# Optimization experiments

Hardware: AMD Instinct MI355X
Metric: run time of the kernel (lower is better)

## Reference

```python
import jax, jax.numpy as jnp
import numpy as np

NUM_GROUPS = 32
EPS = 1e-5

def setup_inputs() -> dict:
    key = jax.random.key(0)
    ks = jax.random.split(key, 10)
    N, C, H, W = 4, 128, 64, 64
    x = jax.random.normal(ks[0], (N, C, H, W), dtype=jnp.float32)
    # GroupNorm affine params
    gn_scale = jnp.ones((C,), dtype=jnp.float32)
    gn_bias = jnp.zeros((C,), dtype=jnp.float32)
    # 1x1 conv weights [out, in] (xavier_uniform scale)
    lim = float(np.sqrt(6.0 / (C + C)))
    wq = jax.random.uniform(ks[1], (C, C), minval=-lim, maxval=lim, dtype=jnp.float32)
    wk = jax.random.uniform(ks[2], (C, C), minval=-lim, maxval=lim, dtype=jnp.float32)
    wv = jax.random.uniform(ks[3], (C, C), minval=-lim, maxval=lim, dtype=jnp.float32)
    wp = jax.random.uniform(ks[4], (C, C), minval=-lim, maxval=lim, dtype=jnp.float32) * 1e-5
    bq = jnp.zeros((C,), dtype=jnp.float32)
    bk = jnp.zeros((C,), dtype=jnp.float32)
    bv = jnp.zeros((C,), dtype=jnp.float32)
    bp = jnp.zeros((C,), dtype=jnp.float32)
    return {"x": x, "gn_scale": gn_scale, "gn_bias": gn_bias,
            "wq": wq, "bq": bq, "wk": wk, "bk": bk,
            "wv": wv, "bv": bv, "wp": wp, "bp": bp}

def _group_norm(x, scale, bias):
    # x: [N, C, H, W]
    N, C, H, W = x.shape
    g = x.reshape(N, NUM_GROUPS, C // NUM_GROUPS, H, W)
    mean = g.mean(axis=(2, 3, 4), keepdims=True)
    var = g.var(axis=(2, 3, 4), keepdims=True)
    g = (g - mean) * jax.lax.rsqrt(var + EPS)
    x = g.reshape(N, C, H, W)
    return x * scale[None, :, None, None] + bias[None, :, None, None]

def reference(x, gn_scale, gn_bias, wq, bq, wk, bk, wv, bv, wp, bp):
    N, C, H, W = x.shape
    h = _group_norm(x, gn_scale, gn_bias)
    # flatten spatial to tokens: [N, HW, C]
    ht = h.reshape(N, C, H * W).transpose(0, 2, 1)
    q = jnp.einsum('nlc,oc->nlo', ht, wq) + bq
    k = jnp.einsum('nlc,oc->nlo', ht, wk) + bk
    v = jnp.einsum('nlc,oc->nlo', ht, wv) + bv
    score = jnp.einsum('nqc,nkc->nqk', q, k) * (C ** -0.5)  # [N, HW, HW]
    attn = jax.nn.softmax(score, axis=-1)
    out = jnp.einsum('nqk,nkc->nqc', attn, v)  # [N, HW, C]
    out = jnp.einsum('nlc,oc->nlo', out, wp) + bp
    out = out.transpose(0, 2, 1).reshape(N, C, H, W)
    return x + out
```

## Files before the change

### kernel.cpp

```cpp
#include <hip/hip_runtime.h>

#define HW 4096
#define CCH 128
#define NB 4

typedef short bf16x8 __attribute__((ext_vector_type(8)));
typedef float f32x4 __attribute__((ext_vector_type(4)));

__device__ __forceinline__ unsigned short f2bf(float f){
  union { float fv; unsigned u; } v; v.fv = f;
  unsigned r = v.u + 0x7fffu + ((v.u >> 16) & 1u);
  return (unsigned short)(r >> 16);
}
__device__ __forceinline__ float bf2f(unsigned short u){
  return __uint_as_float(((unsigned)u) << 16);
}
__device__ __forceinline__ f32x4 mfma16(bf16x8 a, bf16x8 b, f32x4 c){
  return __builtin_amdgcn_mfma_f32_16x16x32_bf16(a, b, c, 0, 0, 0);
}
__device__ __forceinline__ void gll16(const void* g, void* l){
  __builtin_amdgcn_global_load_lds(
      (const __attribute__((address_space(1))) unsigned*)g,
      (__attribute__((address_space(3))) unsigned*)l, 16, 0, 0);
}

__global__ __launch_bounds__(256) void gn_stats_k(const float* __restrict__ x,
    float* __restrict__ stats,
    const float* __restrict__ wq, const float* __restrict__ wk,
    const float* __restrict__ wv, const float* __restrict__ wp,
    unsigned short* __restrict__ wqb, unsigned short* __restrict__ wkb,
    unsigned short* __restrict__ wvb, unsigned short* __restrict__ wpb){
  int tid = threadIdx.x;
  if (tid < 128){
    int f4 = blockIdx.x * 128 + tid;
    int m = f4 >> 12, e = f4 & 4095;
    const float* s4 = (m == 0) ? wq : ((m == 1) ? wk : ((m == 2) ? wv : wp));
    unsigned short* d4 = (m == 0) ? wqb : ((m == 1) ? wkb : ((m == 2) ? wvb : wpb));
    float4 v = *(const float4*)(s4 + e * 4);
    ushort4 b; b.x = f2bf(v.x); b.y = f2bf(v.y); b.z = f2bf(v.z); b.w = f2bf(v.w);
    *(ushort4*)(d4 + e * 4) = b;
  }
  int gid = blockIdx.x;
  const float4* p = (const float4*)(x + (size_t)gid * 16384);
  float s = 0.f, q = 0.f;
  #pragma unroll
  for (int i = 0; i < 16; i++){
    float4 v = p[tid + 256 * i];
    s += v.x + v.y + v.z + v.w;
    q += v.x * v.x + v.y * v.y + v.z * v.z + v.w * v.w;
  }
  #pragma unroll
  for (int d = 1; d < 64; d <<= 1){ s += __shfl_xor(s, d); q += __shfl_xor(q, d); }
  __shared__ float red[8];
  int w = tid >> 6;
  if ((tid & 63) == 0){ red[2 * w] = s; red[2 * w + 1] = q; }
  __syncthreads();
  if (tid == 0){
    float S = red[0] + red[2] + red[4] + red[6];
    float Q = red[1] + red[3] + red[5] + red[7];
    float mean = S * (1.f / 16384.f);
    float var  = Q * (1.f / 16384.f) - mean * mean;
    stats[2 * gid]     = mean;
    stats[2 * gid + 1] = rsqrtf(var + 1e-5f);
  }
}

__global__ __launch_bounds__(256) void gn_apply_k(const float* __restrict__ x,
    const float* __restrict__ stats, const float* __restrict__ sc,
    const float* __restrict__ bi, unsigned short* __restrict__ ht){
  int n = blockIdx.y, l0 = blockIdx.x * 32, tid = threadIdx.x;
  __shared__ __align__(16) unsigned short hs[32][136];
  #pragma unroll
  for (int i = 0; i < 16; i++){
    int c = (tid >> 5) + 8 * i;
    int l = tid & 31;
    float v = x[((size_t)(n * CCH + c)) * HW + l0 + l];
    int grp = n * 32 + (c >> 2);
    float r = (v - stats[2 * grp]) * stats[2 * grp + 1] * sc[c] + bi[c];
    hs[l][c] = f2bf(r);
  }
  __syncthreads();
  #pragma unroll
  for (int i = 0; i < 2; i++){
    int ch = tid + 256 * i;
    int l = ch >> 4, cb = (ch & 15) * 8;
    *(uint4*)&ht[((size_t)(n * HW) + l0 + l) * CCH + cb] = *(const uint4*)&hs[l][cb];
  }
}

__global__ __launch_bounds__(256, 3) void qkv_k(const unsigned short* __restrict__ ht,
    const unsigned short* __restrict__ wqb, const unsigned short* __restrict__ wkb,
    const unsigned short* __restrict__ wvb,
    const float* __restrict__ bq, const float* __restrict__ bk,
    const float* __restrict__ bv,
    unsigned short* __restrict__ Qg, unsigned short* __restrict__ Kg,
    unsigned short* __restrict__ Vt){
  int n = blockIdx.y, l0 = blockIdx.x * 64, m = blockIdx.z, tid = threadIdx.x;
  int w = tid >> 6, lane = tid & 63, l15 = lane & 15, g = lane >> 4;
  __shared__ __align__(16) char lds[49152];
  char* hA = lds;
  char* WB = lds + 16384;
  const unsigned short* wsrc = (m == 0) ? wqb : ((m == 1) ? wkb : wvb);
  const float* bsrc = (m == 0) ? bq : ((m == 1) ? bk : bv);
  {
    const char* hb = (const char*)ht + ((size_t)(n * HW) + l0) * (CCH * 2);
    #pragma unroll
    for (int i = 0; i < 4; i++){
      int T = (4 * w + i) * 64 + lane;
      int row = T >> 4, c16 = (T & 15) ^ (row & 15);
      gll16(hb + row * 256 + c16 * 16, hA + (4 * w + i) * 1024);
    }
    const char* wb2 = (const char*)wsrc;
    #pragma unroll
    for (int i = 0; i < 8; i++){
      int T = (8 * w + i) * 64 + lane;
      int row = T >> 4, c16 = (T & 15) ^ (row & 15);
      gll16(wb2 + row * 256 + c16 * 16, WB + (8 * w + i) * 1024);
    }
  }
  __syncthreads();
  bf16x8 a[4];
  #pragma unroll
  for (int kc = 0; kc < 4; kc++)
    a[kc] = *(const bf16x8*)(hA + (16 * w + l15) * 256 + ((4 * kc + g) ^ l15) * 16);
  f32x4 acc[8];
  #pragma unroll
  for (int ct = 0; ct < 8; ct++) acc[ct] = (f32x4)(0.f);
  #pragma unroll
  for (int ct = 0; ct < 8; ct++)
    #pragma unroll
    for (int kc = 0; kc < 4; kc++){
      bf16x8 bfr = *(const bf16x8*)(WB + (16 * ct + l15) * 256 + ((4 * kc + g) ^ l15) * 16);
      acc[ct] = mfma16(a[kc], bfr, acc[ct]);
    }
  __syncthreads();
  if (m < 2){
    float qs = (m == 0) ? 0.08838834764831845f : 1.0f;
    unsigned short* dst = (m == 0) ? Qg : Kg;
    unsigned short* os = (unsigned short*)(lds + 16384);
    #pragma unroll
    for (int ct = 0; ct < 8; ct++){
      int o = 16 * ct + l15;
      float bias = bsrc[o];
      #pragma unroll
      for (int r = 0; r < 4; r++)
        os[(16 * w + 4 * g + r) * 136 + o] = f2bf((acc[ct][r] + bias) * qs);
    }
    __syncthreads();
    #pragma unroll
    for (int i = 0; i < 4; i++){
      int T = tid + 256 * i;
      int row = T >> 4, cb = T & 15;
      *(uint4*)&dst[((size_t)(n * HW) + l0 + row) * CCH + cb * 8] =
          *(const uint4*)&os[row * 136 + cb * 8];
    }
  } else {
    unsigned short* os = (unsigned short*)(lds + 16384);
    #pragma unroll
    for (int ct = 0; ct < 8; ct++){
      int o = 16 * ct + l15;
      float bias = bsrc[o];
      #pragma unroll
      for (int r = 0; r < 4; r++)
        os[o * 72 + 16 * w + 4 * g + r] = f2bf(acc[ct][r] + bias);
    }
    __syncthreads();
    #pragma unroll
    for (int i = 0; i < 4; i++){
      int T = tid + 256 * i;
      int row = T >> 3, c = T & 7;
      *(uint4*)&Vt[((size_t)(n * CCH) + row) * HW + l0 + c * 8] =
          *(const uint4*)&os[row * 72 + c * 8];
    }
  }
}

__global__ __launch_bounds__(256, 2) void attn_k(const unsigned short* __restrict__ Qg,
    const unsigned short* __restrict__ Kg, const unsigned short* __restrict__ Vt,
    unsigned short* __restrict__ Op, float* __restrict__ Ml, int lsp){
  int nbk = gridDim.x, cpx = nbk >> 3, b = blockIdx.x;
  int swz = (b & 7) * cpx + (b >> 3);
  int q0 = (swz & 63) * 64;
  int rest = swz >> 6;
  int splits = 1 << lsp;
  int sp = rest & (splits - 1);
  int n = rest >> lsp;
  int kvs = HW >> lsp, nt = 64 >> lsp;
  int tid = threadIdx.x;
  int w = tid >> 6, lane = tid & 63, l15 = lane & 15, g = lane >> 4;
  __shared__ __align__(16) char lds[74752];
  char* Pw = lds + 65536 + w * 2304;

  bf16x8 qf[4];
  #pragma unroll
  for (int kc = 0; kc < 4; kc++)
    qf[kc] = *reinterpret_cast<const bf16x8*>(
        &Qg[((size_t)(n * HW) + q0 + 16 * w + l15) * CCH + 32 * kc + 8 * g]);
  f32x4 ov[8];
  #pragma unroll
  for (int i = 0; i < 8; i++) ov[i] = (f32x4)(0.f);
  float mrun[4] = {-3.0e38f, -3.0e38f, -3.0e38f, -3.0e38f};
  float lrun[4] = {0.f, 0.f, 0.f, 0.f};

  const char* kp[4]; const char* vp[4];
  {
    const char* kbase = (const char*)Kg + ((size_t)(n * HW) + sp * kvs) * (CCH * 2);
    const char* vbase = (const char*)Vt + (size_t)(n * CCH) * (HW * 2) + (size_t)sp * kvs * 2;
    #pragma unroll
    for (int i = 0; i < 4; i++){
      int C = (w * 4 + i) * 64 + lane;
      int row = C >> 4, c16 = (C & 15) ^ (row & 15);
      kp[i] = kbase + row * 256 + c16 * 16;
      int vrow = C >> 3, c8 = (C & 7) ^ (vrow & 7);
      vp[i] = vbase + (size_t)vrow * (HW * 2) + c8 * 16;
    }
  }

  #pragma unroll
  for (int i = 0; i < 4; i++) gll16(kp[i], lds + w * 4096 + i * 1024);
  #pragma unroll
  for (int i = 0; i < 4; i++) gll16(vp[i], lds + 16384 + w * 4096 + i * 1024);
  __syncthreads();

  for (int t = 0; t < nt; t++){
    char* cur = lds + ((t & 1) ? 32768 : 0);
    if (t + 1 < nt){
      char* nb = lds + ((t & 1) ? 0 : 32768);
      #pragma unroll
      for (int i = 0; i < 4; i++)
        gll16(kp[i] + (size_t)(t + 1) * 16384, nb + w * 4096 + i * 1024);
      #pragma unroll
      for (int i = 0; i < 4; i++)
        gll16(vp[i] + (size_t)(t + 1) * 128, nb + 16384 + w * 4096 + i * 1024);
    }
    char* Ks = cur; char* Vs = cur + 16384;

    f32x4 s[4];
    __builtin_amdgcn_s_setprio(1);
    #pragma unroll
    for (int ct = 0; ct < 4; ct++){
      f32x4 acc = (f32x4)(0.f);
      #pragma unroll
      for (int kc = 0; kc < 4; kc++){
        bf16x8 kf = *(const bf16x8*)(Ks + (16 * ct + l15) * 256 + ((4 * kc + g) ^ l15) * 16);
        acc = mfma16(qf[kc], kf, acc);
      }
      s[ct] = acc;
    }
    __builtin_amdgcn_s_setprio(0);
    float mx[4];
    #pragma unroll
    for (int r = 0; r < 4; r++)
      mx[r] = fmaxf(fmaxf(s[0][r], s[1][r]), fmaxf(s[2][r], s[3][r]));
    #pragma unroll
    for (int d = 1; d < 16; d <<= 1)
      #pragma unroll
      for (int r = 0; r < 4; r++) mx[r] = fmaxf(mx[r], __shfl_xor(mx[r], d));
    int need = 0;
    #pragma unroll
    for (int r = 0; r < 4; r++) need |= (mx[r] > mrun[r] + 8.0f) ? 1 : 0;
    if (__any(need)){
      float al[4];
      #pragma unroll
      for (int r = 0; r < 4; r++){
        float mn = fmaxf(mrun[r], mx[r]);
        al[r] = __expf(mrun[r] - mn);
        mrun[r] = mn;
        lrun[r] *= al[r];
      }
      #pragma unroll
      for (int ct = 0; ct < 8; ct++)
        #pragma unroll
        for (int r = 0; r < 4; r++) ov[ct][r] *= al[r];
    }
    #pragma unroll
    for (int ct = 0; ct < 4; ct++)
      #pragma unroll
      for (int r = 0; r < 4; r++) s[ct][r] = __expf(s[ct][r] - mrun[r]);
    float rs[4];
    #pragma unroll
    for (int r = 0; r < 4; r++) rs[r] = s[0][r] + s[1][r] + s[2][r] + s[3][r];
    #pragma unroll
    for (int d = 1; d < 16; d <<= 1)
      #pragma unroll
      for (int r = 0; r < 4; r++) rs[r] += __shfl_xor(rs[r], d);
    #pragma unroll
    for (int r = 0; r < 4; r++) lrun[r] += rs[r];

    #pragma unroll
    for (int ct = 0; ct < 4; ct++)
      #pragma unroll
      for (int r = 0; r < 4; r++)
        *(unsigned short*)(Pw + (4 * g + r) * 144 + (16 * ct + l15) * 2) = f2bf(s[ct][r]);
    __builtin_amdgcn_s_setprio(1);
    #pragma unroll
    for (int ct = 0; ct < 8; ct++){
      #pragma unroll
      for (int kc = 0; kc < 2; kc++){
        bf16x8 pa = *(const bf16x8*)(Pw + l15 * 144 + (32 * kc + 8 * g) * 2);
        bf16x8 vf = *(const bf16x8*)(Vs + (16 * ct + l15) * 128 + ((4 * kc + g) ^ (l15 & 7)) * 16);
        ov[ct] = mfma16(pa, vf, ov[ct]);
      }
    }
    __builtin_amdgcn_s_setprio(0);
    __syncthreads();
  }
  size_t obase = (size_t)((sp * NB + n) * HW);
  #pragma unroll
  for (int ct = 0; ct < 8; ct++){
    int o = 16 * ct + l15;
    #pragma unroll
    for (int r = 0; r < 4; r++){
      int l = q0 + 16 * w + 4 * g + r;
      Op[(obase + l) * CCH + o] = f2bf(ov[ct][r]);
    }
  }
  if (l15 == 0){
    #pragma unroll
    for (int r = 0; r < 4; r++){
      int l = q0 + 16 * w + 4 * g + r;
      Ml[(obase + l) * 2]     = mrun[r];
      Ml[(obase + l) * 2 + 1] = lrun[r];
    }
  }
}

__global__ __launch_bounds__(256) void projout_k(const unsigned short* __restrict__ Op,
    const float* __restrict__ Ml, const unsigned short* __restrict__ wpb,
    const float* __restrict__ bp, const float* __restrict__ x,
    float* __restrict__ out, int splits){
  int n = blockIdx.y, l0 = blockIdx.x * 32, tid = threadIdx.x;
  int w = tid >> 6, lane = tid & 63, l15 = lane & 15, g = lane >> 4;
  __shared__ __align__(16) unsigned short hs[32][136];
  __shared__ __align__(16) char WB[32768];
  {
    const char* wb2 = (const char*)wpb;
    #pragma unroll
    for (int i = 0; i < 8; i++){
      int T = (8 * w + i) * 64 + lane;
      int row = T >> 4, c16 = (T & 15) ^ (row & 15);
      gll16(wb2 + row * 256 + c16 * 16, WB + (8 * w + i) * 1024);
    }
  }
  const size_t SSTR = (size_t)NB * HW;
  #pragma unroll
  for (int i = 0; i < 2; i++){
    int T = tid + 256 * i;
    int row = T >> 4, cb = (T & 15) * 8;
    size_t gl = (size_t)n * HW + l0 + row;
    float mv = -3.0e38f;
    #pragma unroll
    for (int s = 0; s < 4; s++)
      if (s < splits) mv = fmaxf(mv, Ml[(s * SSTR + gl) * 2]);
    float fa[8];
    #pragma unroll
    for (int j = 0; j < 8; j++) fa[j] = 0.f;
    float denom = 0.f;
    #pragma unroll
    for (int s = 0; s < 4; s++){
      if (s < splits){
        float wgt = __expf(Ml[(s * SSTR + gl) * 2] - mv);
        denom += wgt * Ml[(s * SSTR + gl) * 2 + 1];
        uint4 a = *(const uint4*)&Op[(s * SSTR + gl) * CCH + cb];
        const unsigned short* au = (const unsigned short*)&a;
        #pragma unroll
        for (int j = 0; j < 8; j++) fa[j] += wgt * bf2f(au[j]);
      }
    }
    float inv = 1.f / denom;
    #pragma unroll
    for (int j = 0; j < 8; j++) hs[row][cb + j] = f2bf(fa[j] * inv);
  }
  __syncthreads();
  int rt = w & 1, cg = w >> 1;
  bf16x8 a[4];
  #pragma unroll
  for (int kc = 0; kc < 4; kc++)
    a[kc] = *reinterpret_cast<const bf16x8*>(&hs[16 * rt + l15][32 * kc + 8 * g]);
  f32x4 acc[4];
  #pragma unroll
  for (int ci = 0; ci < 4; ci++) acc[ci] = (f32x4)(0.f);
  #pragma unroll
  for (int ci = 0; ci < 4; ci++){
    int o = 16 * (cg * 4 + ci) + l15;
    #pragma unroll
    for (int kc = 0; kc < 4; kc++){
      bf16x8 bfr = *(const bf16x8*)(WB + o * 256 + ((4 * kc + g) ^ l15) * 16);
      acc[ci] = mfma16(a[kc], bfr, acc[ci]);
    }
  }
  #pragma unroll
  for (int ci = 0; ci < 4; ci++){
    int o = 16 * (cg * 4 + ci) + l15;
    float bias = bp[o];
    size_t base = ((size_t)(n * CCH) + o) * HW + l0 + 16 * rt + 4 * g;
    float4 xr = *(const float4*)&x[base];
    float4 res;
    res.x = xr.x + acc[ci][0] + bias;
    res.y = xr.y + acc[ci][1] + bias;
    res.z = xr.z + acc[ci][2] + bias;
    res.w = xr.w + acc[ci][3] + bias;
    *(float4*)&out[base] = res;
  }
}

extern "C" void kernel_launch(void* const* d_in, const int* in_sizes, int n_in,
                              void* d_out, int out_size, void* d_ws, size_t ws_size,
                              hipStream_t stream){
  const float* x    = (const float*)d_in[0];
  const float* gnsc = (const float*)d_in[1];
  const float* gnb  = (const float*)d_in[2];
  const float* wq   = (const float*)d_in[3];
  const float* bq   = (const float*)d_in[4];
  const float* wk   = (const float*)d_in[5];
  const float* bk   = (const float*)d_in[6];
  const float* wv   = (const float*)d_in[7];
  const float* bv   = (const float*)d_in[8];
  const float* wp   = (const float*)d_in[9];
  const float* bp   = (const float*)d_in[10];
  float* out = (float*)d_out;

  char* ws = (char*)d_ws;
  const size_t BUF = (size_t)NB * HW * CCH * sizeof(unsigned short);
  const size_t WOFF = 4096;
  const size_t HTOFF = WOFF + 4 * 32768;
  const size_t NEED4 = HTOFF + 8 * BUF + (size_t)4 * NB * HW * 2 * sizeof(float);
  const int lsp = (ws_size >= NEED4) ? 2 : 1;
  const int splits = 1 << lsp;

  float* stats        = (float*)ws;
  unsigned short* wqb = (unsigned short*)(ws + WOFF);
  unsigned short* wkb = (unsigned short*)(ws + WOFF + 32768);
  unsigned short* wvb = (unsigned short*)(ws + WOFF + 65536);
  unsigned short* wpb = (unsigned short*)(ws + WOFF + 98304);
  unsigned short* ht  = (unsigned short*)(ws + HTOFF);
  unsigned short* Qg  = (unsigned short*)(ws + HTOFF + BUF);
  unsigned short* Kg  = (unsigned short*)(ws + HTOFF + 2 * BUF);
  unsigned short* Vt  = (unsigned short*)(ws + HTOFF + 3 * BUF);
  unsigned short* Op  = (unsigned short*)(ws + HTOFF + 4 * BUF);
  float*          Ml  = (float*)(ws + HTOFF + 4 * BUF + (size_t)splits * BUF);

  gn_stats_k<<<128, 256, 0, stream>>>(x, stats, wq, wk, wv, wp, wqb, wkb, wvb, wpb);
  gn_apply_k<<<dim3(128, NB), 256, 0, stream>>>(x, stats, gnsc, gnb, ht);
  qkv_k<<<dim3(64, NB, 3), 256, 0, stream>>>(ht, wqb, wkb, wvb, bq, bk, bv, Qg, Kg, Vt);
  attn_k<<<dim3(64 * NB * splits), 256, 0, stream>>>(Qg, Kg, Vt, Op, Ml, lsp);
  projout_k<<<dim3(128, NB), 256, 0, stream>>>(Op, Ml, wpb, bp, x, out, splits);
}
```

Baseline: 184.4 us.

## Fuse GroupNorm into QKV via grid flag barrier, widen attention query tiles

Folds GroupNorm statistics, normalization and weight casting into the QKV projection kernel. Per-tile partial sums go to a buffer, and blocks meet at a device-wide spin barrier on magic flags. This removes two launches and the normalized-activation round trip through global memory. The attention kernel now processes 128 queries per block, with each wave holding two 16-row query subtiles so every K/V fragment loaded from LDS is reused twice; it also swaps MFMA operand order and packs P with v_cvt_pk_bf16_f32. Risks: the flags are never reset, so on repeated calls the barrier can pass before the current partials are written, and the spin barrier depends on all 768 blocks being resident at once.

Measured after the change: 241.6 us. 31.0% more time.

```diff
diff --git a/kernel.cpp b/kernel.cpp
--- a/kernel.cpp
+++ b/kernel.cpp
@@ -3,6 +3,7 @@
 #define HW 4096
 #define CCH 128
 #define NB 4
+#define MAGIC 0x5A17C0DEu
 
 typedef short bf16x8 __attribute__((ext_vector_type(8)));
 typedef float f32x4 __attribute__((ext_vector_type(4)));
@@ -18,104 +19,117 @@
 __device__ __forceinline__ f32x4 mfma16(bf16x8 a, bf16x8 b, f32x4 c){
   return __builtin_amdgcn_mfma_f32_16x16x32_bf16(a, b, c, 0, 0, 0);
 }
+__device__ __forceinline__ unsigned cvt_pk(float a, float b){
+  unsigned r;
+  asm("v_cvt_pk_bf16_f32 %0, %1, %2" : "=v"(r) : "v"(a), "v"(b));
+  return r;
+}
 __device__ __forceinline__ void gll16(const void* g, void* l){
   __builtin_amdgcn_global_load_lds(
       (const __attribute__((address_space(1))) unsigned*)g,
       (__attribute__((address_space(3))) unsigned*)l, 16, 0, 0);
 }
 
-__global__ __launch_bounds__(256) void gn_stats_k(const float* __restrict__ x,
-    float* __restrict__ stats,
+__global__ __launch_bounds__(256, 3) void fused_k(const float* __restrict__ x,
+    const float* __restrict__ sc, const float* __restrict__ bi,
     const float* __restrict__ wq, const float* __restrict__ wk,
     const float* __restrict__ wv, const float* __restrict__ wp,
-    unsigned short* __restrict__ wqb, unsigned short* __restrict__ wkb,
-    unsigned short* __restrict__ wvb, unsigned short* __restrict__ wpb){
-  int tid = threadIdx.x;
-  if (tid < 128){
-    int f4 = blockIdx.x * 128 + tid;
-    int m = f4 >> 12, e = f4 & 4095;
-    const float* s4 = (m == 0) ? wq : ((m == 1) ? wk : ((m == 2) ? wv : wp));
-    unsigned short* d4 = (m == 0) ? wqb : ((m == 1) ? wkb : ((m == 2) ? wvb : wpb));
-    float4 v = *(const float4*)(s4 + e * 4);
-    ushort4 b; b.x = f2bf(v.x); b.y = f2bf(v.y); b.z = f2bf(v.z); b.w = f2bf(v.w);
-    *(ushort4*)(d4 + e * 4) = b;
-  }
-  int gid = blockIdx.x;
-  const float4* p = (const float4*)(x + (size_t)gid * 16384);
-  float s = 0.f, q = 0.f;
-  #pragma unroll
-  for (int i = 0; i < 16; i++){
-    float4 v = p[tid + 256 * i];
-    s += v.x + v.y + v.z + v.w;
-    q += v.x * v.x + v.y * v.y + v.z * v.z + v.w * v.w;
-  }
-  #pragma unroll
-  for (int d = 1; d < 64; d <<= 1){ s += __shfl_xor(s, d); q += __shfl_xor(q, d); }
-  __shared__ float red[8];
-  int w = tid >> 6;
-  if ((tid & 63) == 0){ red[2 * w] = s; red[2 * w + 1] = q; }
-  __syncthreads();
-  if (tid == 0){
-    float S = red[0] + red[2] + red[4] + red[6];
-    float Q = red[1] + red[3] + red[5] + red[7];
-    float mean = S * (1.f / 16384.f);
-    float var  = Q * (1.f / 16384.f) - mean * mean;
-    stats[2 * gid]     = mean;
-    stats[2 * gid + 1] = rsqrtf(var + 1e-5f);
-  }
-}
-
-__global__ __launch_bounds__(256) void gn_apply_k(const float* __restrict__ x,
-    const float* __restrict__ stats, const float* __restrict__ sc,
-    const float* __restrict__ bi, unsigned short* __restrict__ ht){
-  int n = blockIdx.y, l0 = blockIdx.x * 32, tid = threadIdx.x;
-  __shared__ __align__(16) unsigned short hs[32][136];
-  #pragma unroll
-  for (int i = 0; i < 16; i++){
-    int c = (tid >> 5) + 8 * i;
-    int l = tid & 31;
-    float v = x[((size_t)(n * CCH + c)) * HW + l0 + l];
-    int grp = n * 32 + (c >> 2);
-    float r = (v - stats[2 * grp]) * stats[2 * grp + 1] * sc[c] + bi[c];
-    hs[l][c] = f2bf(r);
-  }
-  __syncthreads();
-  #pragma unroll
-  for (int i = 0; i < 2; i++){
-    int ch = tid + 256 * i;
-    int l = ch >> 4, cb = (ch & 15) * 8;
-    *(uint4*)&ht[((size_t)(n * HW) + l0 + l) * CCH + cb] = *(const uint4*)&hs[l][cb];
-  }
-}
-
-__global__ __launch_bounds__(256, 3) void qkv_k(const unsigned short* __restrict__ ht,
-    const unsigned short* __restrict__ wqb, const unsigned short* __restrict__ wkb,
-    const unsigned short* __restrict__ wvb,
     const float* __restrict__ bq, const float* __restrict__ bk,
     const float* __restrict__ bv,
+    unsigned* __restrict__ flag, float* __restrict__ part,
+    unsigned short* __restrict__ wqb, unsigned short* __restrict__ wkb,
+    unsigned short* __restrict__ wvb, unsigned short* __restrict__ wpb,
     unsigned short* __restrict__ Qg, unsigned short* __restrict__ Kg,
     unsigned short* __restrict__ Vt){
-  int n = blockIdx.y, l0 = blockIdx.x * 64, m = blockIdx.z, tid = threadIdx.x;
+  int lt = blockIdx.x, n = blockIdx.y, m = blockIdx.z, tid = threadIdx.x;
+  int l0 = lt * 64;
   int w = tid >> 6, lane = tid & 63, l15 = lane & 15, g = lane >> 4;
-  __shared__ __align__(16) char lds[49152];
+  __shared__ __align__(16) char lds[49408];
   char* hA = lds;
   char* WB = lds + 16384;
+  float2* sm = (float2*)(lds + 49152);
+
+  float4 xv[8];
+  #pragma unroll
+  for (int i = 0; i < 8; i++){
+    int c = (tid >> 4) + 16 * i, l4 = tid & 15;
+    xv[i] = *(const float4*)&x[((size_t)(n * CCH + c)) * HW + l0 + l4 * 4];
+  }
+  if (m == 0){
+    #pragma unroll
+    for (int i = 0; i < 8; i++){
+      float s = xv[i].x + xv[i].y + xv[i].z + xv[i].w;
+      float q = xv[i].x * xv[i].x + xv[i].y * xv[i].y +
+                xv[i].z * xv[i].z + xv[i].w * xv[i].w;
+      #pragma unroll
+      for (int d = 1; d < 64; d <<= 1){ s += __shfl_xor(s, d); q += __shfl_xor(q, d); }
+      if (lane == 0){
+        int grp = w + 4 * i;
+        *(float2*)&part[((size_t)(n * 32 + grp) * 64 + lt) * 2] = make_float2(s, q);
+      }
+    }
+    int b64 = lt + 64 * n;
+    int idx = b64 * 256 + tid;
+    int mat = idx >> 14, e = idx & 16383;
+    const float* srcw = (mat == 0) ? wq : ((mat == 1) ? wk : ((mat == 2) ? wv : wp));
+    unsigned short* dstw = (mat == 0) ? wqb : ((mat == 1) ? wkb : ((mat == 2) ? wvb : wpb));
+    dstw[e] = f2bf(srcw[e]);
+  }
+  __syncthreads();
+  if (m == 0 && tid == 0)
+    __hip_atomic_store(&flag[lt + 64 * n], MAGIC, __ATOMIC_RELEASE,
+                       __HIP_MEMORY_SCOPE_AGENT);
+  {
+    unsigned it = 0;
+    while (__hip_atomic_load(&flag[tid], __ATOMIC_ACQUIRE,
+                             __HIP_MEMORY_SCOPE_AGENT) != MAGIC){
+      if (++it > 4000000u) break;
+      __builtin_amdgcn_s_sleep(2);
+    }
+  }
+  __syncthreads();
+
   const unsigned short* wsrc = (m == 0) ? wqb : ((m == 1) ? wkb : wvb);
   const float* bsrc = (m == 0) ? bq : ((m == 1) ? bk : bv);
   {
-    const char* hb = (const char*)ht + ((size_t)(n * HW) + l0) * (CCH * 2);
-    #pragma unroll
-    for (int i = 0; i < 4; i++){
-      int T = (4 * w + i) * 64 + lane;
-      int row = T >> 4, c16 = (T & 15) ^ (row & 15);
-      gll16(hb + row * 256 + c16 * 16, hA + (4 * w + i) * 1024);
-    }
     const char* wb2 = (const char*)wsrc;
     #pragma unroll
     for (int i = 0; i < 8; i++){
       int T = (8 * w + i) * 64 + lane;
       int row = T >> 4, c16 = (T & 15) ^ (row & 15);
       gll16(wb2 + row * 256 + c16 * 16, WB + (8 * w + i) * 1024);
+    }
+  }
+  {
+    int g2 = tid >> 3, k = tid & 7;
+    float s = 0.f, q = 0.f;
+    #pragma unroll
+    for (int j = 0; j < 8; j++){
+      float2 p = *(const float2*)&part[((size_t)(n * 32 + g2) * 64 + k * 8 + j) * 2];
+      s += p.x; q += p.y;
+    }
+    #pragma unroll
+    for (int d = 1; d < 8; d <<= 1){ s += __shfl_xor(s, d); q += __shfl_xor(q, d); }
+    if (k == 0){
+      float mean = s * (1.f / 16384.f);
+      float var  = q * (1.f / 16384.f) - mean * mean;
+      sm[g2] = make_float2(mean, rsqrtf(var + 1e-5f));
+    }
+  }
+  __syncthreads();
+  #pragma unroll
+  for (int i = 0; i < 8; i++){
+    int c = (tid >> 4) + 16 * i, l4 = tid & 15;
+    float2 st = sm[c >> 2];
+    float scl = st.y * sc[c];
+    float off = bi[c] - st.x * scl;
+    float rv[4] = { xv[i].x * scl + off, xv[i].y * scl + off,
+                    xv[i].z * scl + off, xv[i].w * scl + off };
+    #pragma unroll
+    for (int j = 0; j < 4; j++){
+      int l = l4 * 4 + j;
+      int slot = (c >> 3) ^ (l & 15);
+      *(unsigned short*)(hA + l * 256 + slot * 16 + ((c & 7) << 1)) = f2bf(rv[j]);
     }
   }
   __syncthreads();
@@ -180,27 +194,30 @@
     unsigned short* __restrict__ Op, float* __restrict__ Ml, int lsp){
   int nbk = gridDim.x, cpx = nbk >> 3, b = blockIdx.x;
   int swz = (b & 7) * cpx + (b >> 3);
-  int q0 = (swz & 63) * 64;
-  int rest = swz >> 6;
+  int qt = swz & 31;
+  int rest = swz >> 5;
   int splits = 1 << lsp;
   int sp = rest & (splits - 1);
   int n = rest >> lsp;
-  int kvs = HW >> lsp, nt = 64 >> lsp;
+  int q0 = qt * 128;
+  int kvs = HW >> lsp;
+  int nt = kvs >> 6;
   int tid = threadIdx.x;
   int w = tid >> 6, lane = tid & 63, l15 = lane & 15, g = lane >> 4;
   __shared__ __align__(16) char lds[74752];
   char* Pw = lds + 65536 + w * 2304;
 
-  bf16x8 qf[4];
-  #pragma unroll
-  for (int kc = 0; kc < 4; kc++)
-    qf[kc] = *reinterpret_cast<const bf16x8*>(
-        &Qg[((size_t)(n * HW) + q0 + 16 * w + l15) * CCH + 32 * kc + 8 * g]);
-  f32x4 ov[8];
-  #pragma unroll
-  for (int i = 0; i < 8; i++) ov[i] = (f32x4)(0.f);
-  float mrun[4] = {-3.0e38f, -3.0e38f, -3.0e38f, -3.0e38f};
-  float lrun[4] = {0.f, 0.f, 0.f, 0.f};
+  int qb = q0 + w * 32;
+  bf16x8 qf0[4], qf1[4];
+  #pragma unroll
+  for (int kc = 0; kc < 4; kc++){
+    qf0[kc] = *(const bf16x8*)&Qg[((size_t)(n * HW) + qb + l15) * CCH + 32 * kc + 8 * g];
+    qf1[kc] = *(const bf16x8*)&Qg[((size_t)(n * HW) + qb + 16 + l15) * CCH + 32 * kc + 8 * g];
+  }
+  f32x4 ov0[8], ov1[8];
+  #pragma unroll
+  for (int i = 0; i < 8; i++){ ov0[i] = (f32x4)(0.f); ov1[i] = (f32x4)(0.f); }
+  float mr0 = -3.0e38f, lr0 = 0.f, mr1 = -3.0e38f, lr1 = 0.f;
 
   const char* kp[4]; const char* vp[4];
   {
@@ -209,119 +226,134 @@
     #pragma unroll
     for (int i = 0; i < 4; i++){
       int C = (w * 4 + i) * 64 + lane;
-      int row = C >> 4, c16 = (C & 15) ^ (row & 15);
-      kp[i] = kbase + row * 256 + c16 * 16;
-      int vrow = C >> 3, c8 = (C & 7) ^ (vrow & 7);
-      vp[i] = vbase + (size_t)vrow * (HW * 2) + c8 * 16;
-    }
-  }
-
-  #pragma unroll
-  for (int i = 0; i < 4; i++) gll16(kp[i], lds + w * 4096 + i * 1024);
-  #pragma unroll
-  for (int i = 0; i < 4; i++) gll16(vp[i], lds + 16384 + w * 4096 + i * 1024);
+      int kr = C >> 4, ks = (C & 15) ^ (kr & 15);
+      kp[i] = kbase + kr * 256 + ks * 16;
+      int vr = C >> 3, c8 = (C & 7) ^ (vr & 7);
+      vp[i] = vbase + (size_t)vr * (HW * 2) + c8 * 16;
+    }
+  }
+  #pragma unroll
+  for (int i = 0; i < 4; i++){
+    gll16(kp[i], lds + w * 4096 + i * 1024);
+    gll16(vp[i], lds + 16384 + w * 4096 + i * 1024);
+  }
   __syncthreads();
 
   for (int t = 0; t < nt; t++){
-    char* cur = lds + ((t & 1) ? 32768 : 0);
+    char* cur = lds + ((t & 1) << 15);
     if (t + 1 < nt){
-      char* nb = lds + ((t & 1) ? 0 : 32768);
-      #pragma unroll
-      for (int i = 0; i < 4; i++)
+      char* nb = lds + (((t + 1) & 1) << 15);
+      #pragma unroll
+      for (int i = 0; i < 4; i++){
         gll16(kp[i] + (size_t)(t + 1) * 16384, nb + w * 4096 + i * 1024);
-      #pragma unroll
-      for (int i = 0; i < 4; i++)
-        gll16(vp[i] + (size_t)(t + 1) * 128, nb + 16384 + w * 4096 + i * 1024);
+        gll16(vp[i] + (size_t)(t + 1) * 128,   nb + 16384 + w * 4096 + i * 1024);
+      }
     }
     char* Ks = cur; char* Vs = cur + 16384;
 
-    f32x4 s[4];
+    f32x4 s0[4], s1[4];
     __builtin_amdgcn_s_setprio(1);
     #pragma unroll
     for (int ct = 0; ct < 4; ct++){
-      f32x4 acc = (f32x4)(0.f);
+      f32x4 a0 = (f32x4)(0.f), a1 = (f32x4)(0.f);
       #pragma unroll
       for (int kc = 0; kc < 4; kc++){
-        bf16x8 kf = *(const bf16x8*)(Ks + (16 * ct + l15) * 256 + ((4 * kc + g) ^ l15) * 16);
-        acc = mfma16(qf[kc], kf, acc);
-      }
-      s[ct] = acc;
+        bf16x8 kf = *(const bf16x8*)(Ks + (16 * ct + l15) * 256 + (((4 * kc + g) ^ l15) << 4));
+        a0 = mfma16(kf, qf0[kc], a0);
+        a1 = mfma16(kf, qf1[kc], a1);
+      }
+      s0[ct] = a0; s1[ct] = a1;
     }
     __builtin_amdgcn_s_setprio(0);
-    float mx[4];
-    #pragma unroll
-    for (int r = 0; r < 4; r++)
-      mx[r] = fmaxf(fmaxf(s[0][r], s[1][r]), fmaxf(s[2][r], s[3][r]));
-    #pragma unroll
-    for (int d = 1; d < 16; d <<= 1)
-      #pragma unroll
-      for (int r = 0; r < 4; r++) mx[r] = fmaxf(mx[r], __shfl_xor(mx[r], d));
-    int need = 0;
-    #pragma unroll
-    for (int r = 0; r < 4; r++) need |= (mx[r] > mrun[r] + 8.0f) ? 1 : 0;
-    if (__any(need)){
-      float al[4];
+
+    float mx0 = -3.0e38f, mx1 = -3.0e38f;
+    #pragma unroll
+    for (int ct = 0; ct < 4; ct++)
       #pragma unroll
       for (int r = 0; r < 4; r++){
-        float mn = fmaxf(mrun[r], mx[r]);
-        al[r] = __expf(mrun[r] - mn);
-        mrun[r] = mn;
-        lrun[r] *= al[r];
-      }
+        mx0 = fmaxf(mx0, s0[ct][r]);
+        mx1 = fmaxf(mx1, s1[ct][r]);
+      }
+    mx0 = fmaxf(mx0, __shfl_xor(mx0, 16)); mx0 = fmaxf(mx0, __shfl_xor(mx0, 32));
+    mx1 = fmaxf(mx1, __shfl_xor(mx1, 16)); mx1 = fmaxf(mx1, __shfl_xor(mx1, 32));
+    if (__any(mx0 > mr0 + 8.0f)){
+      float mn = fmaxf(mr0, mx0);
+      float al = __expf(mr0 - mn);
+      mr0 = mn; lr0 *= al;
       #pragma unroll
       for (int ct = 0; ct < 8; ct++)
         #pragma unroll
-        for (int r = 0; r < 4; r++) ov[ct][r] *= al[r];
-    }
+        for (int r = 0; r < 4; r++) ov0[ct][r] *= al;
+    }
+    if (__any(mx1 > mr1 + 8.0f)){
+      float mn = fmaxf(mr1, mx1);
+      float al = __expf(mr1 - mn);
+      mr1 = mn; lr1 *= al;
+      #pragma unroll
+      for (int ct = 0; ct < 8; ct++)
+        #pragma unroll
+        for (int r = 0; r < 4; r++) ov1[ct][r] *= al;
+    }
+    float rs0 = 0.f, rs1 = 0.f;
     #pragma unroll
     for (int ct = 0; ct < 4; ct++)
       #pragma unroll
-      for (int r = 0; r < 4; r++) s[ct][r] = __expf(s[ct][r] - mrun[r]);
-    float rs[4];
-    #pragma unroll
-    for (int r = 0; r < 4; r++) rs[r] = s[0][r] + s[1][r] + s[2][r] + s[3][r];
-    #pragma unroll
-    for (int d = 1; d < 16; d <<= 1)
-      #pragma unroll
-      for (int r = 0; r < 4; r++) rs[r] += __shfl_xor(rs[r], d);
-    #pragma unroll
-    for (int r = 0; r < 4; r++) lrun[r] += rs[r];
-
+      for (int r = 0; r < 4; r++){
+        float e0 = __expf(s0[ct][r] - mr0); s0[ct][r] = e0; rs0 += e0;
+        float e1 = __expf(s1[ct][r] - mr1); s1[ct][r] = e1; rs1 += e1;
+      }
+    rs0 += __shfl_xor(rs0, 16); rs0 += __shfl_xor(rs0, 32); lr0 += rs0;
+    rs1 += __shfl_xor(rs1, 16); rs1 += __shfl_xor(rs1, 32); lr1 += rs1;
+
+    bf16x8 pb0[2], pb1[2];
     #pragma unroll
     for (int ct = 0; ct < 4; ct++)
       #pragma unroll
-      for (int r = 0; r < 4; r++)
-        *(unsigned short*)(Pw + (4 * g + r) * 144 + (16 * ct + l15) * 2) = f2bf(s[ct][r]);
+      for (int h = 0; h < 2; h++)
+        *(unsigned*)(Pw + l15 * 144 + (8 * ct + 2 * g + h) * 4) =
+            cvt_pk(s0[ct][2 * h], s0[ct][2 * h + 1]);
+    #pragma unroll
+    for (int kc = 0; kc < 2; kc++)
+      pb0[kc] = *(const bf16x8*)(Pw + l15 * 144 + (16 * kc + 4 * g) * 4);
+    #pragma unroll
+    for (int ct = 0; ct < 4; ct++)
+      #pragma unroll
+      for (int h = 0; h < 2; h++)
+        *(unsigned*)(Pw + l15 * 144 + (8 * ct + 2 * g + h) * 4) =
+            cvt_pk(s1[ct][2 * h], s1[ct][2 * h + 1]);
+    #pragma unroll
+    for (int kc = 0; kc < 2; kc++)
+      pb1[kc] = *(const bf16x8*)(Pw + l15 * 144 + (16 * kc + 4 * g) * 4);
+
     __builtin_amdgcn_s_setprio(1);
     #pragma unroll
     for (int ct = 0; ct < 8; ct++){
+      int row = 16 * ct + l15;
       #pragma unroll
       for (int kc = 0; kc < 2; kc++){
-        bf16x8 pa = *(const bf16x8*)(Pw + l15 * 144 + (32 * kc + 8 * g) * 2);
-        bf16x8 vf = *(const bf16x8*)(Vs + (16 * ct + l15) * 128 + ((4 * kc + g) ^ (l15 & 7)) * 16);
-        ov[ct] = mfma16(pa, vf, ov[ct]);
+        bf16x8 vf = *(const bf16x8*)(Vs + row * 128 + (((4 * kc + g) ^ (l15 & 7)) << 4));
+        ov0[ct] = mfma16(vf, pb0[kc], ov0[ct]);
+        ov1[ct] = mfma16(vf, pb1[kc], ov1[ct]);
       }
     }
     __builtin_amdgcn_s_setprio(0);
     __syncthreads();
   }
   size_t obase = (size_t)((sp * NB + n) * HW);
+  size_t qr0 = obase + qb + l15, qr1 = qr0 + 16;
   #pragma unroll
   for (int ct = 0; ct < 8; ct++){
-    int o = 16 * ct + l15;
-    #pragma unroll
-    for (int r = 0; r < 4; r++){
-      int l = q0 + 16 * w + 4 * g + r;
-      Op[(obase + l) * CCH + o] = f2bf(ov[ct][r]);
-    }
-  }
-  if (l15 == 0){
-    #pragma unroll
-    for (int r = 0; r < 4; r++){
-      int l = q0 + 16 * w + 4 * g + r;
-      Ml[(obase + l) * 2]     = mrun[r];
-      Ml[(obase + l) * 2 + 1] = lrun[r];
-    }
+    ushort4 p0, p1;
+    p0.x = f2bf(ov0[ct][0]); p0.y = f2bf(ov0[ct][1]);
+    p0.z = f2bf(ov0[ct][2]); p0.w = f2bf(ov0[ct][3]);
+    p1.x = f2bf(ov1[ct][0]); p1.y = f2bf(ov1[ct][1]);
+    p1.z = f2bf(ov1[ct][2]); p1.w = f2bf(ov1[ct][3]);
+    *(ushort4*)&Op[qr0 * CCH + 16 * ct + 4 * g] = p0;
+    *(ushort4*)&Op[qr1 * CCH + 16 * ct + 4 * g] = p1;
+  }
+  if (g == 0){
+    Ml[qr0 * 2] = mr0; Ml[qr0 * 2 + 1] = lr0;
+    Ml[qr1 * 2] = mr1; Ml[qr1 * 2 + 1] = lr1;
   }
 }
 
@@ -422,27 +454,27 @@
 
   char* ws = (char*)d_ws;
   const size_t BUF = (size_t)NB * HW * CCH * sizeof(unsigned short);
-  const size_t WOFF = 4096;
-  const size_t HTOFF = WOFF + 4 * 32768;
-  const size_t NEED4 = HTOFF + 8 * BUF + (size_t)4 * NB * HW * 2 * sizeof(float);
+  const size_t PARTOFF = 4096;
+  const size_t WOFF2 = PARTOFF + 65536;
+  const size_t QOFF = 204800;
+  const size_t NEED4 = QOFF + 7 * BUF + (size_t)4 * NB * HW * 2 * sizeof(float);
   const int lsp = (ws_size >= NEED4) ? 2 : 1;
   const int splits = 1 << lsp;
 
-  float* stats        = (float*)ws;
-  unsigned short* wqb = (unsigned short*)(ws + WOFF);
-  unsigned short* wkb = (unsigned short*)(ws + WOFF + 32768);
-  unsigned short* wvb = (unsigned short*)(ws + WOFF + 65536);
-  unsigned short* wpb = (unsigned short*)(ws + WOFF + 98304);
-  unsigned short* ht  = (unsigned short*)(ws + HTOFF);
-  unsigned short* Qg  = (unsigned short*)(ws + HTOFF + BUF);
-  unsigned short* Kg  = (unsigned short*)(ws + HTOFF + 2 * BUF);
-  unsigned short* Vt  = (unsigned short*)(ws + HTOFF + 3 * BUF);
-  unsigned short* Op  = (unsigned short*)(ws + HTOFF + 4 * BUF);
-  float*          Ml  = (float*)(ws + HTOFF + 4 * BUF + (size_t)splits * BUF);
-
-  gn_stats_k<<<128, 256, 0, stream>>>(x, stats, wq, wk, wv, wp, wqb, wkb, wvb, wpb);
-  gn_apply_k<<<dim3(128, NB), 256, 0, stream>>>(x, stats, gnsc, gnb, ht);
-  qkv_k<<<dim3(64, NB, 3), 256, 0, stream>>>(ht, wqb, wkb, wvb, bq, bk, bv, Qg, Kg, Vt);
-  attn_k<<<dim3(64 * NB * splits), 256, 0, stream>>>(Qg, Kg, Vt, Op, Ml, lsp);
+  unsigned* flag      = (unsigned*)ws;
+  float* part         = (float*)(ws + PARTOFF);
+  unsigned short* wqb = (unsigned short*)(ws + WOFF2);
+  unsigned short* wkb = (unsigned short*)(ws + WOFF2 + 32768);
+  unsigned short* wvb = (unsigned short*)(ws + WOFF2 + 65536);
+  unsigned short* wpb = (unsigned short*)(ws + WOFF2 + 98304);
+  unsigned short* Qg  = (unsigned short*)(ws + QOFF);
+  unsigned short* Kg  = (unsigned short*)(ws + QOFF + BUF);
+  unsigned short* Vt  = (unsigned short*)(ws + QOFF + 2 * BUF);
+  unsigned short* Op  = (unsigned short*)(ws + QOFF + 3 * BUF);
+  float*          Ml  = (float*)(ws + QOFF + 3 * BUF + (size_t)splits * BUF);
+
+  fused_k<<<dim3(64, NB, 3), 256, 0, stream>>>(x, gnsc, gnb, wq, wk, wv, wp,
+      bq, bk, bv, flag, part, wqb, wkb, wvb, wpb, Qg, Kg, Vt);
+  attn_k<<<dim3(32 * NB * splits), 256, 0, stream>>>(Qg, Kg, Vt, Op, Ml, lsp);
   projout_k<<<dim3(128, NB), 256, 0, stream>>>(Op, Ml, wpb, bp, x, out, splits);
 }
```
